# Performance work log

Hardware: AMD Instinct MI355X
Metric: run time of the kernel (lower is better)

Reference implementation:

```python
import jax, jax.numpy as jnp
import numpy as np

N_NODES = 100000
N_EDGES = 1600000
IN_F = 256
OUT_F = 128


def setup_inputs() -> dict:
    key = jax.random.key(0)
    k1, k2, k3, k4, k5 = jax.random.split(key, 5)
    x = jax.random.normal(k1, (N_NODES, IN_F), dtype=jnp.float32)
    edge_rows = jax.random.randint(k2, (N_EDGES,), 0, N_NODES, dtype=jnp.int32)
    edge_cols = jax.random.randint(k3, (N_EDGES,), 0, N_NODES, dtype=jnp.int32)
    edge_vals = jax.random.uniform(k4, (N_EDGES,), dtype=jnp.float32)
    # glorot init for weight, zeros for bias (matches reset_parameters)
    limit = float(np.sqrt(6.0 / (IN_F + OUT_F)))
    weight = jax.random.uniform(k5, (IN_F, OUT_F), dtype=jnp.float32,
                                minval=-limit, maxval=limit)
    bias = jnp.zeros((OUT_F,), dtype=jnp.float32)
    return {"x": x, "edge_rows": edge_rows, "edge_cols": edge_cols,
            "edge_vals": edge_vals, "weight": weight, "bias": bias}


def reference(x, edge_rows, edge_cols, edge_vals, weight, bias):
    # dense projection: [N, in] @ [in, out] -> [N, out]
    h = x @ weight
    # spmm(adj, h): out[r] = sum_{edges e with row r} vals[e] * h[col[e]]
    msgs = edge_vals[:, None] * h[edge_cols]          # [E, out]
    agg = jax.ops.segment_sum(msgs, edge_rows, num_segments=N_NODES)
    return agg + bias
```

## Files before the change

kernel.cpp:

```cpp
#include <hip/hip_runtime.h>


typedef __attribute__((ext_vector_type(8))) short short8;
typedef __attribute__((ext_vector_type(4))) float floatx4;

#define WT_K 264
#define GM_NODES 128
#define BSHIFT 6
#define BROWS 64
#define CAP 256
#define OVFCAP 65536
#define XCC_GETREG_IMM 6164

static __device__ __forceinline__ uint f2bf(float x) {
  uint u = __float_as_uint(x);
  return (u + 0x7fffu + ((u >> 16) & 1u)) >> 16;
}

__global__ __launch_bounds__(256) void conv_w(const float* __restrict__ w,
                                              ushort* __restrict__ wt) {
  const int f = blockIdx.x;
  const int k = threadIdx.x;
  wt[f * WT_K + k] = (ushort)f2bf(w[k * 128 + f]);
}

__global__ __launch_bounds__(256) void gemm_mfma(const float* __restrict__ x,
                                                 const ushort* __restrict__ wt,
                                                 ushort* __restrict__ h,
                                                 int n_nodes) {
  __shared__ ushort lw[128 * WT_K];
  __shared__ ushort xa[GM_NODES * 40];
  const int t = threadIdx.x;
  const int lane = t & 63;
  const int wq = t >> 6;
  const int quad = lane >> 4;
  const int l15 = lane & 15;
  const int row0 = blockIdx.x * GM_NODES;

  {
    const uint4* src = (const uint4*)wt;
    uint4* dst = (uint4*)lw;
    for (int i = t; i < (128 * WT_K * 2) / 16; i += 256) dst[i] = src[i];
  }

  floatx4 acc[2][8];
#pragma unroll
  for (int nt = 0; nt < 2; ++nt)
#pragma unroll
    for (int mt = 0; mt < 8; ++mt) acc[nt][mt] = (floatx4){0.f, 0.f, 0.f, 0.f};

  float4 cur[4];
#pragma unroll
  for (int i = 0; i < 4; ++i) {
    const int idx = i * 256 + t;
    const int row = idx >> 3, kq = idx & 7;
    const int gr = row0 + row;
    cur[i] = (gr < n_nodes) ? *(const float4*)&x[(size_t)gr * 256 + kq * 4]
                            : make_float4(0.f, 0.f, 0.f, 0.f);
  }

  for (int kc = 0; kc < 8; ++kc) {
#pragma unroll
    for (int i = 0; i < 4; ++i) {
      const int idx = i * 256 + t;
      const int row = idx >> 3, kq = idx & 7;
      uint2 p;
      p.x = f2bf(cur[i].x) | (f2bf(cur[i].y) << 16);
      p.y = f2bf(cur[i].z) | (f2bf(cur[i].w) << 16);
      *(uint2*)&xa[row * 40 + kq * 4] = p;
    }
    __syncthreads();

    float4 nxt[4];
    if (kc < 7) {
#pragma unroll
      for (int i = 0; i < 4; ++i) {
        const int idx = i * 256 + t;
        const int row = idx >> 3, kq = idx & 7;
        const int gr = row0 + row;
        nxt[i] = (gr < n_nodes)
                     ? *(const float4*)&x[(size_t)gr * 256 + (kc + 1) * 32 + kq * 4]
                     : make_float4(0.f, 0.f, 0.f, 0.f);
      }
    }

    short8 bfr[2];
    bfr[0] = *(const short8*)&xa[(wq * 32 + l15) * 40 + quad * 8];
    bfr[1] = *(const short8*)&xa[(wq * 32 + 16 + l15) * 40 + quad * 8];
#pragma unroll
    for (int mt = 0; mt < 8; ++mt) {
      const short8 afr =
          *(const short8*)&lw[(mt * 16 + l15) * WT_K + kc * 32 + quad * 8];
      acc[0][mt] = __builtin_amdgcn_mfma_f32_16x16x32_bf16(afr, bfr[0],
                                                           acc[0][mt], 0, 0, 0);
      acc[1][mt] = __builtin_amdgcn_mfma_f32_16x16x32_bf16(afr, bfr[1],
                                                           acc[1][mt], 0, 0, 0);
    }
    __syncthreads();
#pragma unroll
    for (int i = 0; i < 4; ++i) cur[i] = nxt[i];
  }

#pragma unroll
  for (int nt = 0; nt < 2; ++nt) {
    const int node = row0 + wq * 32 + nt * 16 + l15;
    if (node < n_nodes) {
#pragma unroll
      for (int mt = 0; mt < 8; ++mt) {
        uint2 p;
        p.x = f2bf(acc[nt][mt][0]) | (f2bf(acc[nt][mt][1]) << 16);
        p.y = f2bf(acc[nt][mt][2]) | (f2bf(acc[nt][mt][3]) << 16);
        *(uint2*)&h[(size_t)node * 128 + mt * 16 + quad * 4] = p;
      }
    }
  }
}

__global__ __launch_bounds__(256) void fill_xcd(
    const int* __restrict__ erows, const int* __restrict__ ecols,
    const float* __restrict__ evals, int* __restrict__ cursor3,
    int2* __restrict__ bcv, int* __restrict__ ovf_cnt,
    int4* __restrict__ ovf, int n_edges) {
  int i = blockIdx.x * 256 + threadIdx.x;
  if (i >= n_edges) return;
  const int xcd = (int)(__builtin_amdgcn_s_getreg(XCC_GETREG_IMM)) & 7;
  const int r = erows[i];
  const int c = ecols[i];
  const float v = evals[i];
  const int reg = ((r >> BSHIFT) << 3) | xcd;
  const int pos = atomicAdd(&cursor3[reg], 1);
  if (pos < CAP) {
    int2 p;
    p.x = c | ((r & (BROWS - 1)) << 17);
    p.y = __float_as_int(v);
    bcv[(size_t)reg * CAP + pos] = p;
  } else {
    int op = atomicAdd(ovf_cnt, 1);
    if (op < OVFCAP) {
      int4 q; q.x = r; q.y = c; q.z = __float_as_int(v); q.w = 0;
      ovf[op] = q;
    }
  }
}

__global__ __launch_bounds__(256) void sort_gather(
    const ushort* __restrict__ h, const int* __restrict__ cursor3,
    const int2* __restrict__ bcv, const float* __restrict__ bias,
    float* __restrict__ out, int n_nodes) {
  __shared__ int2 buf[8 * CAP];
  __shared__ int cnt[BROWS], start[BROWS], cur[BROWS];
  __shared__ int scnt[8];
  const int b = blockIdx.x;
  const int t = threadIdx.x;
  if (t < 8) scnt[t] = min(cursor3[b * 8 + t], CAP);
  if (t < BROWS) cnt[t] = 0;
  __syncthreads();

#pragma unroll
  for (int x = 0; x < 8; ++x) {
    const int n = scnt[x];
    const int2* src = &bcv[(size_t)(b * 8 + x) * CAP];
    for (int i = t; i < n; i += 256) atomicAdd(&cnt[((uint)src[i].x) >> 17], 1);
  }
  __syncthreads();

  if (t < BROWS) {
    int c = cnt[t];
    int s = c;
#pragma unroll
    for (int off = 1; off < 64; off <<= 1) {
      int u = __shfl_up(s, off, 64);
      if (t >= off) s += u;
    }
    start[t] = s - c;
    cur[t] = s - c;
  }
  __syncthreads();

#pragma unroll
  for (int x = 0; x < 8; ++x) {
    const int n = scnt[x];
    const int2* src = &bcv[(size_t)(b * 8 + x) * CAP];
    for (int i = t; i < n; i += 256) {
      int2 rec = src[i];
      int pos = atomicAdd(&cur[((uint)rec.x) >> 17], 1);
      buf[pos] = rec;
    }
  }
  __syncthreads();

  const int lane = t & 63;
  const int w = t >> 6;
  const float2 bv = ((const float2*)bias)[lane];
  for (int rr = w * 16; rr < w * 16 + 16; ++rr) {
    const int node = b * BROWS + rr;
    if (node >= n_nodes) break;
    float2 acc = bv;
    int p = start[rr];
    const int p1 = start[rr] + cnt[rr];
    for (; p + 4 <= p1; p += 4) {
      int2 e0 = buf[p + 0];
      int2 e1 = buf[p + 1];
      int2 e2 = buf[p + 2];
      int2 e3 = buf[p + 3];
      uint u0 = ((const uint*)(h + (size_t)(e0.x & 0x1FFFF) * 128))[lane];
      uint u1 = ((const uint*)(h + (size_t)(e1.x & 0x1FFFF) * 128))[lane];
      uint u2 = ((const uint*)(h + (size_t)(e2.x & 0x1FFFF) * 128))[lane];
      uint u3 = ((const uint*)(h + (size_t)(e3.x & 0x1FFFF) * 128))[lane];
      float v0 = __int_as_float(e0.y), v1 = __int_as_float(e1.y);
      float v2 = __int_as_float(e2.y), v3 = __int_as_float(e3.y);
      acc.x += v0 * __uint_as_float(u0 << 16);
      acc.y += v0 * __uint_as_float(u0 & 0xffff0000u);
      acc.x += v1 * __uint_as_float(u1 << 16);
      acc.y += v1 * __uint_as_float(u1 & 0xffff0000u);
      acc.x += v2 * __uint_as_float(u2 << 16);
      acc.y += v2 * __uint_as_float(u2 & 0xffff0000u);
      acc.x += v3 * __uint_as_float(u3 << 16);
      acc.y += v3 * __uint_as_float(u3 & 0xffff0000u);
    }
    for (; p < p1; ++p) {
      int2 ev = buf[p];
      float v = __int_as_float(ev.y);
      uint u = ((const uint*)(h + (size_t)(ev.x & 0x1FFFF) * 128))[lane];
      acc.x += v * __uint_as_float(u << 16);
      acc.y += v * __uint_as_float(u & 0xffff0000u);
    }
    ((float2*)(out + (size_t)node * 128))[lane] = acc;
  }
}

__global__ __launch_bounds__(256) void ovf_scatter(
    const ushort* __restrict__ h, const int* __restrict__ ovf_cnt,
    const int4* __restrict__ ovf, float* __restrict__ out) {
  const int n = min(*ovf_cnt, OVFCAP);
  const int lane = threadIdx.x & 63;
  const int wid = (blockIdx.x * 256 + threadIdx.x) >> 6;
  const int nw = gridDim.x * 4;
  for (int e = wid; e < n; e += nw) {
    int4 rec = ovf[e];
    float v = __int_as_float(rec.z);
    uint u = ((const uint*)(h + (size_t)rec.y * 128))[lane];
    float* op = out + (size_t)rec.x * 128 + lane * 2;
    atomicAdd(op, v * __uint_as_float(u << 16));
    atomicAdd(op + 1, v * __uint_as_float(u & 0xffff0000u));
  }
}

__global__ __launch_bounds__(256) void init_bias(float* __restrict__ out,
                                                 const float* __restrict__ bias,
                                                 int n4) {
  int i = blockIdx.x * 256 + threadIdx.x;
  if (i < n4) {
    float4 b = ((const float4*)bias)[i & 31];
    ((float4*)out)[i] = b;
  }
}

__global__ __launch_bounds__(256) void scatter_edges(
    const ushort* __restrict__ h, const int* __restrict__ erows,
    const int* __restrict__ ecols, const float* __restrict__ evals,
    float* __restrict__ out, int n_edges) {
  int e = blockIdx.x * 4 + (threadIdx.x >> 6);
  if (e >= n_edges) return;
  int lane = threadIdx.x & 63;
  int row = erows[e];
  int col = ecols[e];
  float v = evals[e];
  uint u = ((const uint*)(h + (size_t)col * 128))[lane];
  float* op = out + (size_t)row * 128 + lane * 2;
  atomicAdd(op, v * __uint_as_float(u << 16));
  atomicAdd(op + 1, v * __uint_as_float(u & 0xffff0000u));
}

extern "C" void kernel_launch(void* const* d_in, const int* in_sizes, int n_in,
                              void* d_out, int out_size, void* d_ws, size_t ws_size,
                              hipStream_t stream) {
  const float* x     = (const float*)d_in[0];
  const int*   erows = (const int*)d_in[1];
  const int*   ecols = (const int*)d_in[2];
  const float* evals = (const float*)d_in[3];
  const float* w     = (const float*)d_in[4];
  const float* bias  = (const float*)d_in[5];
  float* out = (float*)d_out;

  const int n_nodes = in_sizes[0] / 256;
  const int n_edges = in_sizes[1];
  const int nb_buckets = (n_nodes + BROWS - 1) >> BSHIFT;
  const int nb8 = nb_buckets * 8;

  char* ws = (char*)d_ws;
  size_t off = 0;
  ushort* h  = (ushort*)(ws + off);  off += ((size_t)n_nodes * 128 * 2 + 15) & ~15ull;
  ushort* wt = (ushort*)(ws + off);  off += ((size_t)128 * WT_K * 2 + 15) & ~15ull;
  int* cursor3 = (int*)(ws + off);   off += ((size_t)(nb8 + 1) * 4 + 15) & ~15ull;
  int2* bcv    = (int2*)(ws + off);  off += (size_t)nb8 * CAP * 8;
  int4* ovf    = (int4*)(ws + off);  off += (size_t)OVFCAP * 16;
  const bool bucket_ok = (off <= ws_size) && (n_nodes <= (1 << 17));
  int* ovf_cnt = cursor3 + nb8;

  conv_w<<<128, 256, 0, stream>>>(w, wt);
  const int gemm_blocks = (n_nodes + GM_NODES - 1) / GM_NODES;
  gemm_mfma<<<gemm_blocks, 256, 0, stream>>>(x, wt, h, n_nodes);

  if (bucket_ok) {
    hipMemsetAsync(cursor3, 0, (size_t)(nb8 + 1) * 4, stream);
    const int eblocks = (n_edges + 255) / 256;
    fill_xcd<<<eblocks, 256, 0, stream>>>(erows, ecols, evals, cursor3, bcv,
                                          ovf_cnt, ovf, n_edges);
    sort_gather<<<nb_buckets, 256, 0, stream>>>(h, cursor3, bcv, bias, out,
                                                n_nodes);
    ovf_scatter<<<32, 256, 0, stream>>>(h, ovf_cnt, ovf, out);
  } else {
    const int n4 = out_size / 4;
    init_bias<<<(n4 + 255) / 256, 256, 0, stream>>>(out, bias, n4);
    scatter_edges<<<(n_edges + 3) / 4, 256, 0, stream>>>(h, erows, ecols, evals,
                                                         out, n_edges);
  }
}
```

Before: 349.8 us.

## Pad bucket cursors, use XCD-major bucket layout, shrink capacity, add nontemporal loads

Edge bucket cursors are padded so each sits on its own 64-byte line, removing false sharing between atomics. Buckets and cursors are reordered XCD-major so each XCD's writes land in a contiguous region. Per-bucket capacity drops from 256 to 192, which shrinks LDS use and the staging buffer but raises the chance of spilling into the slower overflow path. Streaming edge and bucket reads use nontemporal loads to avoid polluting cache.

```diff
diff --git a/kernel.cpp b/kernel.cpp
--- a/kernel.cpp
+++ b/kernel.cpp
@@ -3,12 +3,14 @@
 
 typedef __attribute__((ext_vector_type(8))) short short8;
 typedef __attribute__((ext_vector_type(4))) float floatx4;
+typedef __attribute__((ext_vector_type(2))) int intv2;
 
 #define WT_K 264
 #define GM_NODES 128
 #define BSHIFT 6
 #define BROWS 64
-#define CAP 256
+#define CAP 192
+#define CSH 4
 #define OVFCAP 65536
 #define XCC_GETREG_IMM 6164
 
@@ -118,17 +120,17 @@
 
 __global__ __launch_bounds__(256) void fill_xcd(
     const int* __restrict__ erows, const int* __restrict__ ecols,
-    const float* __restrict__ evals, int* __restrict__ cursor3,
+    const float* __restrict__ evals, int* __restrict__ cursors,
     int2* __restrict__ bcv, int* __restrict__ ovf_cnt,
-    int4* __restrict__ ovf, int n_edges) {
+    int4* __restrict__ ovf, int n_edges, int nb) {
   int i = blockIdx.x * 256 + threadIdx.x;
   if (i >= n_edges) return;
   const int xcd = (int)(__builtin_amdgcn_s_getreg(XCC_GETREG_IMM)) & 7;
-  const int r = erows[i];
-  const int c = ecols[i];
-  const float v = evals[i];
-  const int reg = ((r >> BSHIFT) << 3) | xcd;
-  const int pos = atomicAdd(&cursor3[reg], 1);
+  const int r = __builtin_nontemporal_load(&erows[i]);
+  const int c = __builtin_nontemporal_load(&ecols[i]);
+  const float v = __builtin_nontemporal_load(&evals[i]);
+  const int reg = xcd * nb + (r >> BSHIFT);
+  const int pos = atomicAdd(&cursors[reg << CSH], 1);
   if (pos < CAP) {
     int2 p;
     p.x = c | ((r & (BROWS - 1)) << 17);
@@ -144,22 +146,22 @@
 }
 
 __global__ __launch_bounds__(256) void sort_gather(
-    const ushort* __restrict__ h, const int* __restrict__ cursor3,
+    const ushort* __restrict__ h, const int* __restrict__ cursors,
     const int2* __restrict__ bcv, const float* __restrict__ bias,
-    float* __restrict__ out, int n_nodes) {
+    float* __restrict__ out, int n_nodes, int nb) {
   __shared__ int2 buf[8 * CAP];
   __shared__ int cnt[BROWS], start[BROWS], cur[BROWS];
   __shared__ int scnt[8];
   const int b = blockIdx.x;
   const int t = threadIdx.x;
-  if (t < 8) scnt[t] = min(cursor3[b * 8 + t], CAP);
+  if (t < 8) scnt[t] = min(cursors[(t * nb + b) << CSH], CAP);
   if (t < BROWS) cnt[t] = 0;
   __syncthreads();
 
 #pragma unroll
   for (int x = 0; x < 8; ++x) {
     const int n = scnt[x];
-    const int2* src = &bcv[(size_t)(b * 8 + x) * CAP];
+    const int2* src = &bcv[(size_t)(x * nb + b) * CAP];
     for (int i = t; i < n; i += 256) atomicAdd(&cnt[((uint)src[i].x) >> 17], 1);
   }
   __syncthreads();
@@ -180,9 +182,10 @@
 #pragma unroll
   for (int x = 0; x < 8; ++x) {
     const int n = scnt[x];
-    const int2* src = &bcv[(size_t)(b * 8 + x) * CAP];
+    const intv2* src = (const intv2*)&bcv[(size_t)(x * nb + b) * CAP];
     for (int i = t; i < n; i += 256) {
-      int2 rec = src[i];
+      intv2 rr = __builtin_nontemporal_load(&src[i]);
+      int2 rec; rec.x = rr[0]; rec.y = rr[1];
       int pos = atomicAdd(&cur[((uint)rec.x) >> 17], 1);
       buf[pos] = rec;
     }
@@ -290,25 +293,26 @@
 
   char* ws = (char*)d_ws;
   size_t off = 0;
-  ushort* h  = (ushort*)(ws + off);  off += ((size_t)n_nodes * 128 * 2 + 15) & ~15ull;
-  ushort* wt = (ushort*)(ws + off);  off += ((size_t)128 * WT_K * 2 + 15) & ~15ull;
-  int* cursor3 = (int*)(ws + off);   off += ((size_t)(nb8 + 1) * 4 + 15) & ~15ull;
-  int2* bcv    = (int2*)(ws + off);  off += (size_t)nb8 * CAP * 8;
+  ushort* h  = (ushort*)(ws + off);  off += ((size_t)n_nodes * 128 * 2 + 255) & ~255ull;
+  ushort* wt = (ushort*)(ws + off);  off += ((size_t)128 * WT_K * 2 + 255) & ~255ull;
+  const size_t cur_ints = (((size_t)nb8) << CSH) + 16;
+  int* cursors = (int*)(ws + off);   off += (cur_ints * 4 + 255) & ~255ull;
+  int2* bcv    = (int2*)(ws + off);  off += ((size_t)nb8 * CAP * 8 + 255) & ~255ull;
   int4* ovf    = (int4*)(ws + off);  off += (size_t)OVFCAP * 16;
   const bool bucket_ok = (off <= ws_size) && (n_nodes <= (1 << 17));
-  int* ovf_cnt = cursor3 + nb8;
+  int* ovf_cnt = cursors + (((size_t)nb8) << CSH);
 
   conv_w<<<128, 256, 0, stream>>>(w, wt);
   const int gemm_blocks = (n_nodes + GM_NODES - 1) / GM_NODES;
   gemm_mfma<<<gemm_blocks, 256, 0, stream>>>(x, wt, h, n_nodes);
 
   if (bucket_ok) {
-    hipMemsetAsync(cursor3, 0, (size_t)(nb8 + 1) * 4, stream);
+    hipMemsetAsync(cursors, 0, cur_ints * 4, stream);
     const int eblocks = (n_edges + 255) / 256;
-    fill_xcd<<<eblocks, 256, 0, stream>>>(erows, ecols, evals, cursor3, bcv,
-                                          ovf_cnt, ovf, n_edges);
-    sort_gather<<<nb_buckets, 256, 0, stream>>>(h, cursor3, bcv, bias, out,
-                                                n_nodes);
+    fill_xcd<<<eblocks, 256, 0, stream>>>(erows, ecols, evals, cursors, bcv,
+                                          ovf_cnt, ovf, n_edges, nb_buckets);
+    sort_gather<<<nb_buckets, 256, 0, stream>>>(h, cursors, bcv, bias, out,
+                                                n_nodes, nb_buckets);
     ovf_scatter<<<32, 256, 0, stream>>>(h, ovf_cnt, ovf, out);
   } else {
     const int n4 = out_size / 4;
```

New measurement: 333.6 us. -4.6%, faster.
